# Optimization experiments

Hardware: AMD Instinct MI355X
Metric: run time of the kernel (lower is better)

## Reference

```python
import jax, jax.numpy as jnp
import numpy as np

B, C, N, H = 8, 256, 2048, 4
DIM = C // H
EPS = 1e-5
SLOPE = 0.2


def conv1x1(W, b, x):
    # W: [out, in], x: [B, in, N] -> [B, out, N]
    return jnp.einsum('oc,bcn->bon', W, x) + b[None, :, None]


def setup_inputs() -> dict:
    key = jax.random.key(0)
    ks = jax.random.split(key, 16)
    s = 1.0 / np.sqrt(C)
    s2 = 1.0 / np.sqrt(2 * C)
    return {
        'init_query': jax.random.normal(ks[0], (B, C, N), jnp.float32),
        'key': jax.random.normal(ks[1], (B, C, N), jnp.float32),
        'value': jax.random.normal(ks[2], (B, C, N), jnp.float32),
        'Wq': jax.random.normal(ks[3], (C, C), jnp.float32) * s,
        'bq': jax.random.normal(ks[4], (C,), jnp.float32) * s,
        'Wk': jax.random.normal(ks[5], (C, C), jnp.float32) * s,
        'bk': jax.random.normal(ks[6], (C,), jnp.float32) * s,
        'Wv': jax.random.normal(ks[7], (C, C), jnp.float32) * s,
        'bv': jax.random.normal(ks[8], (C,), jnp.float32) * s,
        'Wm': jax.random.normal(ks[9], (C, C), jnp.float32) * s,
        'bm': jax.random.normal(ks[10], (C,), jnp.float32) * s,
        'W1': jax.random.normal(ks[11], (2 * C, 2 * C), jnp.float32) * s2,
        'b1': jax.random.normal(ks[12], (2 * C,), jnp.float32) * s2,
        'gamma': jnp.ones((2 * C,), jnp.float32),
        'beta': jnp.zeros((2 * C,), jnp.float32),
        'W2': jax.random.normal(ks[13], (C, 2 * C), jnp.float32) * s2,
        'b2': jnp.zeros((C,), jnp.float32),  # nn.init.constant_(bias, 0.0)
    }


def reference(init_query, key, value, Wq, bq, Wk, bk, Wv, bv, Wm, bm, W1, b1, gamma, beta, W2, b2):
    # projections, then view [B, C, N] -> [B, dim, H, N] (dim outermost, matching torch .view)
    q = conv1x1(Wq, bq, init_query).reshape(B, DIM, H, N)
    k = conv1x1(Wk, bk, key).reshape(B, DIM, H, N)
    v = conv1x1(Wv, bv, value).reshape(B, DIM, H, N)
    scores = jnp.einsum('bdhn,bdhm->bhnm', q, k) / jnp.sqrt(jnp.float32(DIM))
    attn = jax.nn.softmax(scores, axis=-1)  # [B, H, N, N]
    x = jnp.einsum('bhnm,bdhm->bdhn', attn, v).reshape(B, C, N)
    x = conv1x1(Wm, bm, x)
    # post_merge: conv1x1 -> BatchNorm1d (training-mode batch stats) -> LeakyReLU(0.2) -> conv1x1
    h = conv1x1(W1, b1, jnp.concatenate([x, init_query], axis=1))  # [B, 2C, N]
    mu = jnp.mean(h, axis=(0, 2), keepdims=True)
    var = jnp.mean(jnp.square(h - mu), axis=(0, 2), keepdims=True)  # biased var, as torch BN
    hn = (h - mu) / jnp.sqrt(var + EPS) * gamma[None, :, None] + beta[None, :, None]
    hn = jnp.where(hn > 0, hn, SLOPE * hn)
    out = conv1x1(W2, b2, hn)
    return (out, attn)
```

## Files before the change

### kernel.cpp

```cpp
#include <hip/hip_runtime.h>
#include <stdint.h>

typedef __bf16 bf16x8 __attribute__((ext_vector_type(8)));
typedef float f32x4 __attribute__((ext_vector_type(4)));

constexpr int NB = 8;
constexpr int NC = 256;
constexpr int NN = 2048;
constexpr int NH = 4;
constexpr int ND = 64;
constexpr int NC2 = 512;
constexpr size_t TND = (size_t)NB * NN * NC;
__device__ constexpr float C2 = 0.125f * 1.4426950408889634f;

__device__ __forceinline__ ushort f2bf(float f) {
  union { float f; uint32_t u; } x; x.f = f;
  return (ushort)((x.u + 0x7FFFu + ((x.u >> 16) & 1u)) >> 16);
}
__device__ __forceinline__ float bf2f(ushort h) {
  union { uint32_t u; float f; } x; x.u = (uint32_t)h << 16;
  return x.f;
}

__device__ __forceinline__ void bar_lds() {
  __builtin_amdgcn_sched_barrier(0);
  asm volatile("s_waitcnt lgkmcnt(0)" ::: "memory");
  __builtin_amdgcn_s_barrier();
  __builtin_amdgcn_sched_barrier(0);
}


__global__ void k_cast_all(const float* __restrict__ Wq, const float* __restrict__ Wk,
                           const float* __restrict__ Wv, const float* __restrict__ Wm,
                           const float* __restrict__ W1, const float* __restrict__ W2,
                           ushort* __restrict__ wqkv, ushort* __restrict__ wm_b,
                           ushort* __restrict__ w1_b, ushort* __restrict__ w2_b) {
  int i = blockIdx.x * 256 + threadIdx.x;
  if (i < 196608) {
    int op = i >> 16, j = i & 65535;
    int r = j >> 8, c = j & 255;
    const float* s = op == 0 ? Wq : op == 1 ? Wk : Wv;
    int orig = op < 2 ? (((r & 63) << 2) | (r >> 6)) : r;
    wqkv[i] = f2bf(s[orig * NC + c]);
  } else if (i < 262144) {
    int j = i - 196608;
    int co = j >> 8, jj = j & 255;
    wm_b[j] = f2bf(Wm[co * NC + (jj & 63) * NH + (jj >> 6)]);
  } else if (i < 524288) {
    int j = i - 262144;
    w1_b[j] = f2bf(W1[j]);
  } else {
    int j = i - 524288;
    w2_b[j] = f2bf(W2[j]);
  }
}

__global__ void k_bn_finalize(const float* __restrict__ stats, const float* __restrict__ gamma,
                              const float* __restrict__ beta, float4* __restrict__ aff) {
  int c = blockIdx.x * 256 + threadIdx.x;
  if (c >= NC2) return;
  const float inv_n = 1.f / (float)(NB * NN);
  float mu  = stats[c * 2] * inv_n;
  float var = stats[c * 2 + 1] * inv_n - mu * mu;
  float isg = gamma[c] * rsqrtf(var + 1e-5f);
  aff[c] = make_float4(mu, isg, beta[c], 0.f);
}


__device__ __forceinline__ bf16x8 ldtile(const ushort* base, int lr, int lg, int fc, int ks) {
  int row = fc * 16 + lr;
  int u = (ks * 4 + lg) ^ (lr & 7);
  return *(const bf16x8*)((const char*)base + row * 128 + u * 16);
}

__global__ __launch_bounds__(256, 4) void k_attn(
    const ushort* __restrict__ qt, const ushort* __restrict__ kt,
    const ushort* __restrict__ vnat, float* __restrict__ attn,
    ushort* __restrict__ xT) {
  __shared__ ushort Kl[2][4096];
  __shared__ ushort Vl[2][4096];
  __shared__ ushort Pl[4096];

  const int tid = threadIdx.x;
  const int lane = tid & 63, w = tid >> 6;
  const int lr = lane & 15, lg = lane >> 4;

  int flat = blockIdx.x;
  int xcd = flat & 7, idx = flat >> 3;
  int z = xcd * 4 + (idx >> 5);
  int r0 = (idx & 31) * 64;
  int b = z >> 2, h = z & 3;

  const ushort* kbase = kt + (size_t)z * NN * ND;
  const ushort* vbase = vnat + ((size_t)b * NC + h) * NN;

  const int sr0 = tid >> 3, sc0 = tid & 7;
  const int sr1 = 32 + sr0;
  const int d0 = sr0 * 128 + ((sc0 ^ (sr0 & 7)) << 4);
  const int d1 = sr1 * 128 + ((sc0 ^ (sr1 & 7)) << 4);

  bf16x8 aq0, aq1;
  {
    const ushort* qp = qt + ((size_t)z * NN + r0 + w * 16 + lr) * ND;
    aq0 = *(const bf16x8*)(qp + lg * 8);
    aq1 = *(const bf16x8*)(qp + 32 + lg * 8);
  }

  uint4 gk0, gk1, gv0, gv1;

  gk0 = *(const uint4*)(kbase + (size_t)sr0 * ND + sc0 * 8);
  gk1 = *(const uint4*)(kbase + (size_t)sr1 * ND + sc0 * 8);
  *(uint4*)((char*)Kl[0] + d0) = gk0;
  *(uint4*)((char*)Kl[0] + d1) = gk1;
  gk0 = *(const uint4*)(kbase + (size_t)(64 + sr0) * ND + sc0 * 8);
  gk1 = *(const uint4*)(kbase + (size_t)(64 + sr1) * ND + sc0 * 8);
  bar_lds();

  float m_ln[4], s_ln[4];
#pragma unroll
  for (int j = 0; j < 4; ++j) { m_ln[j] = -INFINITY; s_ln[j] = 0.f; }

  for (int t = 0; t < 32; ++t) {
    int kb = t & 1;
    if (t < 31) {
      *(uint4*)((char*)Kl[kb ^ 1] + d0) = gk0;
      *(uint4*)((char*)Kl[kb ^ 1] + d1) = gk1;
    }
    if (t < 30) {
      gk0 = *(const uint4*)(kbase + ((size_t)(t + 2) * 64 + sr0) * ND + sc0 * 8);
      gk1 = *(const uint4*)(kbase + ((size_t)(t + 2) * 64 + sr1) * ND + sc0 * 8);
    }
    f32x4 sa[4] = {};
#pragma unroll
    for (int ks = 0; ks < 2; ++ks) {
      bf16x8 aqk = ks ? aq1 : aq0;
#pragma unroll
      for (int fc = 0; fc < 4; ++fc)
        sa[fc] = __builtin_amdgcn_mfma_f32_16x16x32_bf16(aqk, ldtile(Kl[kb], lr, lg, fc, ks), sa[fc], 0, 0, 0);
    }
#pragma unroll
    for (int j = 0; j < 4; ++j) {
      float tm = fmaxf(fmaxf(sa[0][j], sa[1][j]), fmaxf(sa[2][j], sa[3][j]));
      float mn = fmaxf(m_ln[j], tm);
      float mnC = mn * C2;
      float es = exp2f(fmaf(sa[0][j], C2, -mnC)) + exp2f(fmaf(sa[1][j], C2, -mnC))
               + exp2f(fmaf(sa[2][j], C2, -mnC)) + exp2f(fmaf(sa[3][j], C2, -mnC));
      s_ln[j] = s_ln[j] * exp2f(fmaf(m_ln[j], C2, -mnC)) + es;
      m_ln[j] = mn;
    }
    bar_lds();
  }

  float mC[4];
#pragma unroll
  for (int j = 0; j < 4; ++j) {
    float m = m_ln[j];
#pragma unroll
    for (int o = 1; o < 16; o <<= 1) m = fmaxf(m, __shfl_xor(m, o));
    float c = s_ln[j] * exp2f((m_ln[j] - m) * C2);
#pragma unroll
    for (int o = 1; o < 16; o <<= 1) c += __shfl_xor(c, o);
    mC[j] = m * C2 + __log2f(c);
  }

  gk0 = *(const uint4*)(kbase + (size_t)sr0 * ND + sc0 * 8);
  gk1 = *(const uint4*)(kbase + (size_t)sr1 * ND + sc0 * 8);
  gv0 = *(const uint4*)(vbase + (size_t)sr0 * 4 * NN + sc0 * 8);
  gv1 = *(const uint4*)(vbase + (size_t)sr1 * 4 * NN + sc0 * 8);
  *(uint4*)((char*)Kl[0] + d0) = gk0;
  *(uint4*)((char*)Kl[0] + d1) = gk1;
  *(uint4*)((char*)Vl[0] + d0) = gv0;
  *(uint4*)((char*)Vl[0] + d1) = gv1;
  gk0 = *(const uint4*)(kbase + (size_t)(64 + sr0) * ND + sc0 * 8);
  gk1 = *(const uint4*)(kbase + (size_t)(64 + sr1) * ND + sc0 * 8);
  gv0 = *(const uint4*)(vbase + (size_t)sr0 * 4 * NN + 64 + sc0 * 8);
  gv1 = *(const uint4*)(vbase + (size_t)sr1 * 4 * NN + 64 + sc0 * 8);
  bar_lds();

  f32x4 acc[4] = {};
  const int prow = w * 16 + lr;
  char* plb = (char*)Pl;
  for (int t = 0; t < 32; ++t) {
    int kb = t & 1;
    if (t < 31) {
      *(uint4*)((char*)Kl[kb ^ 1] + d0) = gk0;
      *(uint4*)((char*)Kl[kb ^ 1] + d1) = gk1;
      *(uint4*)((char*)Vl[kb ^ 1] + d0) = gv0;
      *(uint4*)((char*)Vl[kb ^ 1] + d1) = gv1;
    }
    if (t < 30) {
      gk0 = *(const uint4*)(kbase + ((size_t)(t + 2) * 64 + sr0) * ND + sc0 * 8);
      gk1 = *(const uint4*)(kbase + ((size_t)(t + 2) * 64 + sr1) * ND + sc0 * 8);
      gv0 = *(const uint4*)(vbase + (size_t)sr0 * 4 * NN + (t + 2) * 64 + sc0 * 8);
      gv1 = *(const uint4*)(vbase + (size_t)sr1 * 4 * NN + (t + 2) * 64 + sc0 * 8);
    }
    f32x4 sa[4] = {};
#pragma unroll
    for (int ks = 0; ks < 2; ++ks) {
      bf16x8 aqk = ks ? aq1 : aq0;
#pragma unroll
      for (int fc = 0; fc < 4; ++fc)
        sa[fc] = __builtin_amdgcn_mfma_f32_16x16x32_bf16(aqk, ldtile(Kl[kb], lr, lg, fc, ks), sa[fc], 0, 0, 0);
    }
#pragma unroll
    for (int fc = 0; fc < 4; ++fc)
#pragma unroll
      for (int j = 0; j < 4; ++j) {
        int row = w * 16 + lg * 4 + j;
        float p = exp2f(fmaf(sa[fc][j], C2, -mC[j]));
        int byte = (row << 7) + ((fc * 16 + lr) << 1);
        byte ^= (row & 7) << 4;
        *(ushort*)(plb + byte) = f2bf(p);
      }
    float* abase = attn + ((size_t)z * NN + r0) * NN + t * 64;
#pragma unroll
    for (int k = 0; k < 4; ++k) {
      int row = w * 16 + lg + k * 4;
      int byte = (row << 7) + (lr << 3);
      byte ^= (row & 7) << 4;
      const ushort* pq = (const ushort*)(plb + byte);
      f32x4 vv = { bf2f(pq[0]), bf2f(pq[1]), bf2f(pq[2]), bf2f(pq[3]) };
      __builtin_nontemporal_store(vv, (f32x4*)(abase + (size_t)row * NN + lr * 4));
    }
#pragma unroll
    for (int ks = 0; ks < 2; ++ks) {
      int abyte = (prow << 7) + ks * 64 + lg * 16;
      abyte ^= (prow & 7) << 4;
      bf16x8 ap = *(const bf16x8*)(plb + abyte);
#pragma unroll
      for (int fc = 0; fc < 4; ++fc)
        acc[fc] = __builtin_amdgcn_mfma_f32_16x16x32_bf16(ap, ldtile(Vl[kb], lr, lg, fc, ks), acc[fc], 0, 0, 0);
    }
    bar_lds();
  }
#pragma unroll
  for (int fc = 0; fc < 4; ++fc)
#pragma unroll
    for (int j = 0; j < 4; ++j) {
      int n = r0 + w * 16 + lg * 4 + j;
      xT[((size_t)b * NN + n) * NC + h * 64 + fc * 16 + lr] = f2bf(acc[fc][j]);
    }
}


enum GemmMode { M_PROJ = 0, M_WM, M_W1, M_W2 };

template <int MODE>
__global__ __launch_bounds__(256) void k_gemm(
    const ushort* __restrict__ A, const ushort* __restrict__ Bm,
    const float* __restrict__ Fa, const float* __restrict__ Fb, const float* __restrict__ Fc,
    const float* __restrict__ b0, const float* __restrict__ b1v, const float* __restrict__ b2v,
    const float4* __restrict__ aff, float* __restrict__ stats,
    float* __restrict__ outf, ushort* __restrict__ outb, ushort* __restrict__ outb2) {
  constexpr int BR = (MODE == M_WM || MODE == M_W2) ? 64 : 128;
  constexpr int BC = 128;
  constexpr int KT = (MODE == M_PROJ || MODE == M_WM) ? 256 : 512;
  constexpr int FR = BR / 32;
  constexpr int FC = 4;
  constexpr int LDL = 72;

  __shared__ ushort ldsU[BR * LDL + BC * LDL];
  ushort* ldsA = ldsU;
  ushort* ldsB = ldsU + BR * LDL;

  const int tid = threadIdx.x;
  const int lane = tid & 63, wave = tid >> 6;
  const int wr = (wave >> 1) * (FR * 16), wc = (wave & 1) * (FC * 16);
  const int lr = lane & 15, lg = lane >> 4, lk = lg * 8;
  const int c0 = blockIdx.x * BC, r0 = blockIdx.y * BR;
  const int op = (MODE == M_PROJ) ? (int)(blockIdx.z >> 3) : 0;
  const size_t z = (MODE == M_PROJ) ? (blockIdx.z & 7) : blockIdx.z;

  auto stage_t = [&](ushort* dst, const float* src) {
    int n = tid & 127, half = tid >> 7;
#pragma unroll
    for (int u = 0; u < 4; ++u) {
      int cg = half + u * 2;
      union { ushort us[8]; uint4 v; } pk;
#pragma unroll
      for (int e = 0; e < 8; ++e)
        pk.us[e] = f2bf(src[(size_t)(cg * 8 + e) * NN + n]);
      *(uint4*)&dst[n * LDL + cg * 8] = pk.v;
    }
  };

  f32x4 acc[FR][FC] = {};

  for (int kk = 0; kk < KT; kk += 64) {
    if constexpr (MODE == M_W1) {
      if (kk < NC) {
        const ushort* src = A + (z * NN + r0) * (size_t)NC + kk;
#pragma unroll
        for (int i = 0; i < BR / 32; ++i) {
          int off = (tid + i * 256) * 8, row = off >> 6, k = off & 63;
          *(uint4*)&ldsA[row * LDL + k] = *(const uint4*)(src + (size_t)row * NC + k);
        }
      } else {
        stage_t(ldsA, Fa + ((size_t)z * NC + (kk - NC)) * NN + r0);
      }
    } else {
      const ushort* src; int ld;
      if constexpr (MODE == M_PROJ)        { src = A + (size_t)op * NC * NC + (size_t)r0 * NC + kk; ld = NC; }
      else if constexpr (MODE == M_WM)     { src = A + (z * NN + r0) * (size_t)NC + kk; ld = NC; }
      else                                  { src = A + (size_t)r0 * NC2 + kk; ld = NC2; }
#pragma unroll
      for (int i = 0; i < BR / 32; ++i) {
        int off = (tid + i * 256) * 8, row = off >> 6, k = off & 63;
        *(uint4*)&ldsA[row * LDL + k] = *(const uint4*)(src + (size_t)row * ld + k);
      }
    }
    if constexpr (MODE == M_PROJ) {
      const float* Fsel = op == 0 ? Fa : op == 1 ? Fb : Fc;
      stage_t(ldsB, Fsel + ((size_t)z * NC + kk) * NN + c0);
    } else if constexpr (MODE == M_W2) {
      const ushort* src = Bm + (z * NN + c0) * (size_t)NC2 + kk;
#pragma unroll
      for (int i = 0; i < BC / 32; ++i) {
        int off = (tid + i * 256) * 8, row = off >> 6, k = off & 63;
        union { ushort u[8]; uint4 v; } t, o;
        t.v = *(const uint4*)(src + (size_t)row * NC2 + k);
#pragma unroll
        for (int e = 0; e < 8; ++e) {
          float4 pr = aff[kk + k + e];
          float y = (bf2f(t.u[e]) - pr.x) * pr.y + pr.z;
          y = y > 0.f ? y : 0.2f * y;
          o.u[e] = f2bf(y);
        }
        *(uint4*)&ldsB[row * LDL + k] = o.v;
      }
    } else {
      const ushort* src; int ld;
      if constexpr (MODE == M_WM)          { src = Bm + (size_t)c0 * NC + kk; ld = NC; }
      else                                  { src = Bm + (size_t)c0 * NC2 + kk; ld = NC2; }
#pragma unroll
      for (int i = 0; i < BC / 32; ++i) {
        int off = (tid + i * 256) * 8, row = off >> 6, k = off & 63;
        *(uint4*)&ldsB[row * LDL + k] = *(const uint4*)(src + (size_t)row * ld + k);
      }
    }
    __syncthreads();
#pragma unroll
    for (int ks = 0; ks < 2; ++ks) {
      bf16x8 afr[FR], bfr[FC];
#pragma unroll
      for (int fr = 0; fr < FR; ++fr)
        afr[fr] = *(const bf16x8*)&ldsA[(wr + fr * 16 + lr) * LDL + ks * 32 + lk];
#pragma unroll
      for (int fc = 0; fc < FC; ++fc)
        bfr[fc] = *(const bf16x8*)&ldsB[(wc + fc * 16 + lr) * LDL + ks * 32 + lk];
#pragma unroll
      for (int fr = 0; fr < FR; ++fr)
#pragma unroll
        for (int fc = 0; fc < FC; ++fc)
          acc[fr][fc] = __builtin_amdgcn_mfma_f32_16x16x32_bf16(afr[fr], bfr[fc], acc[fr][fc], 0, 0, 0);
    }
    __syncthreads();
  }

  if constexpr (MODE == M_PROJ) {
    if (op < 2) {
      const float* bb = op == 0 ? b0 : b1v;
      char* tb = (char*)ldsU;
#pragma unroll
      for (int fr = 0; fr < FR; ++fr)
#pragma unroll
        for (int fc = 0; fc < FC; ++fc) {
          int n_l = wc + fc * 16 + lr;
          int rb = wr + fr * 16 + lg * 4;
          union { ushort u[4]; uint2 v; } pk;
#pragma unroll
          for (int j = 0; j < 4; ++j) {
            int r = r0 + rb + j;
            pk.u[j] = f2bf(acc[fr][fc][j] + bb[((r & 63) << 2) | (r >> 6)]);
          }
          int byte = n_l * 256 + rb * 2;
          byte ^= (n_l & 7) << 4;
          *(uint2*)(tb + byte) = pk.v;
        }
      __syncthreads();
      ushort* dst = outb + (size_t)op * TND;
#pragma unroll
      for (int hh = 0; hh < 2; ++hh) {
        size_t zz = z * 4 + (r0 >> 6) + hh;
#pragma unroll
        for (int u = 0; u < 4; ++u) {
          int seg = u * 256 + tid;
          int n_l = seg >> 3, dd = (seg & 7) * 8;
          int byte = n_l * 256 + (hh * 64 + dd) * 2;
          byte ^= (n_l & 7) << 4;
          uint4 v = *(const uint4*)(tb + byte);
          *(uint4*)(dst + (zz * NN + c0 + n_l) * (size_t)ND + dd) = v;
        }
      }
    } else {
#pragma unroll
      for (int fr = 0; fr < FR; ++fr)
#pragma unroll
        for (int fc = 0; fc < FC; ++fc)
#pragma unroll
          for (int j = 0; j < 4; ++j) {
            int r = r0 + wr + fr * 16 + lg * 4 + j;
            int c = c0 + wc + fc * 16 + lr;
            outb2[(z * NC + r) * (size_t)NN + c] = f2bf(acc[fr][fc][j] + b2v[r]);
          }
    }
    return;
  }

  float sfc[FC], qfc[FC];
#pragma unroll
  for (int fc = 0; fc < FC; ++fc) { sfc[fc] = 0.f; qfc[fc] = 0.f; }
#pragma unroll
  for (int fr = 0; fr < FR; ++fr)
#pragma unroll
    for (int fc = 0; fc < FC; ++fc)
#pragma unroll
      for (int j = 0; j < 4; ++j) {
        int r = r0 + wr + fr * 16 + lg * 4 + j;
        int c = c0 + wc + fc * 16 + lr;
        float v = acc[fr][fc][j];
        if constexpr (MODE == M_WM) {
          v += b0[c];
          outb[(z * NN + r) * (size_t)NC + c] = f2bf(v);
        } else if constexpr (MODE == M_W1) {
          v += b0[c];
          outb[(z * NN + r) * (size_t)NC2 + c] = f2bf(v);
          sfc[fc] += v; qfc[fc] += v * v;
        } else {
          v += b0[r];
          outf[(z * NC + r) * (size_t)NN + c] = v;
        }
      }
  if constexpr (MODE == M_W1) {
#pragma unroll
    for (int fc = 0; fc < FC; ++fc) {
      float s1 = sfc[fc], s2 = qfc[fc];
      s1 += __shfl_xor(s1, 16); s1 += __shfl_xor(s1, 32);
      s2 += __shfl_xor(s2, 16); s2 += __shfl_xor(s2, 32);
      if (lane < 16) {
        int ch = c0 + wc + fc * 16 + lane;
        atomicAdd(&stats[ch * 2],     s1);
        atomicAdd(&stats[ch * 2 + 1], s2);
      }
    }
  }
}


extern "C" void kernel_launch(void* const* d_in, const int* in_sizes, int n_in,
                              void* d_out, int out_size, void* d_ws, size_t ws_size,
                              hipStream_t stream) {
  const float* iq    = (const float*)d_in[0];
  const float* keyi  = (const float*)d_in[1];
  const float* vali  = (const float*)d_in[2];
  const float* Wq = (const float*)d_in[3];  const float* bq = (const float*)d_in[4];
  const float* Wk = (const float*)d_in[5];  const float* bk = (const float*)d_in[6];
  const float* Wv = (const float*)d_in[7];  const float* bv = (const float*)d_in[8];
  const float* Wm = (const float*)d_in[9];  const float* bm = (const float*)d_in[10];
  const float* W1 = (const float*)d_in[11]; const float* b1 = (const float*)d_in[12];
  const float* gamma = (const float*)d_in[13]; const float* beta = (const float*)d_in[14];
  const float* W2 = (const float*)d_in[15]; const float* b2 = (const float*)d_in[16];

  float* out  = (float*)d_out;
  float* attn = out + (size_t)NB * NC * NN;

  uint8_t* cur = (uint8_t*)d_ws;
  auto alloc = [&](size_t bytes) { uint8_t* p = cur; cur += (bytes + 255) & ~(size_t)255; return p; };
  ushort* wqkv  = (ushort*)alloc((size_t)NC * NC * 2 * 3);
  ushort* wm_b  = (ushort*)alloc((size_t)NC * NC * 2);
  ushort* w1_b  = (ushort*)alloc((size_t)NC2 * NC2 * 2);
  ushort* w2_b  = (ushort*)alloc((size_t)NC * NC2 * 2);
  ushort* qtkt  = (ushort*)alloc(TND * 2 * 2);
  ushort* v_nat = (ushort*)alloc(TND * 2);
  ushort* xT    = (ushort*)alloc(TND * 2);
  ushort* xmT   = (ushort*)alloc(TND * 2);
  ushort* hT    = (ushort*)alloc((size_t)NB * NN * NC2 * 2);
  float*  stats = (float*)alloc(NC2 * 2 * 4);
  float4* aff   = (float4*)alloc(NC2 * 16);
  ushort* kt    = qtkt + TND;

  (void)hipMemsetAsync(stats, 0, NC2 * 2 * 4, stream);

  k_cast_all<<<dim3(2560), 256, 0, stream>>>(Wq, Wk, Wv, Wm, W1, W2, wqkv, wm_b, w1_b, w2_b);

  k_gemm<M_PROJ><<<dim3(16, 2, 24), 256, 0, stream>>>(
      wqkv, nullptr, iq, keyi, vali, bq, bk, bv, nullptr, nullptr, nullptr, qtkt, v_nat);

  k_attn<<<dim3(1024), 256, 0, stream>>>(qtkt, kt, v_nat, attn, xT);

  k_gemm<M_WM><<<dim3(2, 32, 8), 256, 0, stream>>>(
      xT, wm_b, nullptr, nullptr, nullptr, bm, nullptr, nullptr, nullptr, nullptr, nullptr, xmT, nullptr);

  k_gemm<M_W1><<<dim3(4, 16, 8), 256, 0, stream>>>(
      xmT, w1_b, iq, nullptr, nullptr, b1, nullptr, nullptr, nullptr, stats, nullptr, hT, nullptr);

  k_bn_finalize<<<dim3(2), 256, 0, stream>>>(stats, gamma, beta, aff);

  k_gemm<M_W2><<<dim3(16, 4, 8), 256, 0, stream>>>(
      w2_b, hT, nullptr, nullptr, nullptr, b2, nullptr, nullptr, aff, nullptr, out, nullptr, nullptr);
}
```

Baseline: 266.4 us.

## Fold merge conv into first post-merge conv and fuse BN finalize into W2 GEMM

Precomputes W1[:, :C] @ Wm (with the head permutation) and the folded bias in the prep kernel, so the separate Wm GEMM over all activations and its intermediate buffer are removed. The BN finalize kernel is dropped: each W2 GEMM block recomputes the per-channel affine from stats into shared memory. This saves one full GEMM pass, a round trip to memory and two launches. In exchange the prep kernel does a small matmul serially per thread, every W2 block repeats the finalize work, and the folded weights are rounded to bf16 directly rather than applied in two steps.

```diff
diff --git a/kernel.cpp b/kernel.cpp
--- a/kernel.cpp
+++ b/kernel.cpp
@@ -30,40 +30,45 @@
 }
 
 
-__global__ void k_cast_all(const float* __restrict__ Wq, const float* __restrict__ Wk,
-                           const float* __restrict__ Wv, const float* __restrict__ Wm,
-                           const float* __restrict__ W1, const float* __restrict__ W2,
-                           ushort* __restrict__ wqkv, ushort* __restrict__ wm_b,
-                           ushort* __restrict__ w1_b, ushort* __restrict__ w2_b) {
-  int i = blockIdx.x * 256 + threadIdx.x;
-  if (i < 196608) {
-    int op = i >> 16, j = i & 65535;
-    int r = j >> 8, c = j & 255;
-    const float* s = op == 0 ? Wq : op == 1 ? Wk : Wv;
-    int orig = op < 2 ? (((r & 63) << 2) | (r >> 6)) : r;
-    wqkv[i] = f2bf(s[orig * NC + c]);
-  } else if (i < 262144) {
-    int j = i - 196608;
-    int co = j >> 8, jj = j & 255;
-    wm_b[j] = f2bf(Wm[co * NC + (jj & 63) * NH + (jj >> 6)]);
-  } else if (i < 524288) {
-    int j = i - 262144;
-    w1_b[j] = f2bf(W1[j]);
+__global__ void k_prep(const float* __restrict__ Wq, const float* __restrict__ Wk,
+                       const float* __restrict__ Wv, const float* __restrict__ Wm,
+                       const float* __restrict__ W1, const float* __restrict__ W2,
+                       const float* __restrict__ bm, const float* __restrict__ b1,
+                       ushort* __restrict__ wqkv, ushort* __restrict__ w2_b,
+                       ushort* __restrict__ wf_b, float* __restrict__ bias_f) {
+  int blk = blockIdx.x, tid = threadIdx.x;
+  if (blk < 1792) {
+    int gid = blk * 256 + tid;
+    if (gid < 196608) {
+      int op = gid >> 16, j = gid & 65535;
+      int r = j >> 8, c = j & 255;
+      const float* s = op == 0 ? Wq : op == 1 ? Wk : Wv;
+      int orig = op < 2 ? (((r & 63) << 2) | (r >> 6)) : r;
+      wqkv[gid] = f2bf(s[orig * NC + c]);
+    } else if (gid < 327680) {
+      int j = gid - 196608;
+      w2_b[j] = f2bf(W2[j]);
+    } else {
+      int j = gid - 327680;
+      int o = j >> 8, co = j & 255;
+      wf_b[o * NC2 + NC + co] = f2bf(W1[o * NC2 + NC + co]);
+    }
   } else {
-    int j = i - 524288;
-    w2_b[j] = f2bf(W2[j]);
-  }
-}
-
-__global__ void k_bn_finalize(const float* __restrict__ stats, const float* __restrict__ gamma,
-                              const float* __restrict__ beta, float4* __restrict__ aff) {
-  int c = blockIdx.x * 256 + threadIdx.x;
-  if (c >= NC2) return;
-  const float inv_n = 1.f / (float)(NB * NN);
-  float mu  = stats[c * 2] * inv_n;
-  float var = stats[c * 2 + 1] * inv_n - mu * mu;
-  float isg = gamma[c] * rsqrtf(var + 1e-5f);
-  aff[c] = make_float4(mu, isg, beta[c], 0.f);
+    int o = blk - 1792;
+    int pc = ((tid & 63) << 2) | (tid >> 6);
+    const float* w1row = W1 + (size_t)o * NC2;
+    float acc = 0.f;
+    for (int co = 0; co < NC; ++co)
+      acc = fmaf(w1row[co], Wm[co * NC + pc], acc);
+    wf_b[o * NC2 + tid] = f2bf(acc);
+    float pb = w1row[tid] * bm[tid];
+#pragma unroll
+    for (int ofs = 1; ofs < 64; ofs <<= 1) pb += __shfl_xor(pb, ofs);
+    __shared__ float red[4];
+    if ((tid & 63) == 0) red[tid >> 6] = pb;
+    __syncthreads();
+    if (tid == 0) bias_f[o] = b1[o] + red[0] + red[1] + red[2] + red[3];
+  }
 }
 
 
@@ -243,23 +248,24 @@
 }
 
 
-enum GemmMode { M_PROJ = 0, M_WM, M_W1, M_W2 };
+enum GemmMode { M_PROJ = 0, M_W1, M_W2 };
 
 template <int MODE>
 __global__ __launch_bounds__(256) void k_gemm(
     const ushort* __restrict__ A, const ushort* __restrict__ Bm,
     const float* __restrict__ Fa, const float* __restrict__ Fb, const float* __restrict__ Fc,
     const float* __restrict__ b0, const float* __restrict__ b1v, const float* __restrict__ b2v,
-    const float4* __restrict__ aff, float* __restrict__ stats,
+    float* __restrict__ stats,
     float* __restrict__ outf, ushort* __restrict__ outb, ushort* __restrict__ outb2) {
-  constexpr int BR = (MODE == M_WM || MODE == M_W2) ? 64 : 128;
+  constexpr int BR = (MODE == M_W2) ? 64 : 128;
   constexpr int BC = 128;
-  constexpr int KT = (MODE == M_PROJ || MODE == M_WM) ? 256 : 512;
+  constexpr int KT = (MODE == M_PROJ) ? 256 : 512;
   constexpr int FR = BR / 32;
   constexpr int FC = 4;
   constexpr int LDL = 72;
 
   __shared__ ushort ldsU[BR * LDL + BC * LDL];
+  __shared__ float4 affl[(MODE == M_W2) ? NC2 : 1];
   ushort* ldsA = ldsU;
   ushort* ldsB = ldsU + BR * LDL;
 
@@ -271,6 +277,17 @@
   const int op = (MODE == M_PROJ) ? (int)(blockIdx.z >> 3) : 0;
   const size_t z = (MODE == M_PROJ) ? (blockIdx.z & 7) : blockIdx.z;
 
+  if constexpr (MODE == M_W2) {
+    const float inv_n = 1.f / (float)(NB * NN);
+    for (int c = tid; c < NC2; c += 256) {
+      float mu  = stats[c * 2] * inv_n;
+      float var = stats[c * 2 + 1] * inv_n - mu * mu;
+      float isg = b1v[c] * rsqrtf(var + 1e-5f);
+      affl[c] = make_float4(mu, isg, b2v[c], 0.f);
+    }
+    __syncthreads();
+  }
+
   auto stage_t = [&](ushort* dst, const float* src) {
     int n = tid & 127, half = tid >> 7;
 #pragma unroll
@@ -300,9 +317,8 @@
       }
     } else {
       const ushort* src; int ld;
-      if constexpr (MODE == M_PROJ)        { src = A + (size_t)op * NC * NC + (size_t)r0 * NC + kk; ld = NC; }
-      else if constexpr (MODE == M_WM)     { src = A + (z * NN + r0) * (size_t)NC + kk; ld = NC; }
-      else                                  { src = A + (size_t)r0 * NC2 + kk; ld = NC2; }
+      if constexpr (MODE == M_PROJ) { src = A + (size_t)op * NC * NC + (size_t)r0 * NC + kk; ld = NC; }
+      else                           { src = A + (size_t)r0 * NC2 + kk; ld = NC2; }
 #pragma unroll
       for (int i = 0; i < BR / 32; ++i) {
         int off = (tid + i * 256) * 8, row = off >> 6, k = off & 63;
@@ -321,7 +337,7 @@
         t.v = *(const uint4*)(src + (size_t)row * NC2 + k);
 #pragma unroll
         for (int e = 0; e < 8; ++e) {
-          float4 pr = aff[kk + k + e];
+          float4 pr = affl[kk + k + e];
           float y = (bf2f(t.u[e]) - pr.x) * pr.y + pr.z;
           y = y > 0.f ? y : 0.2f * y;
           o.u[e] = f2bf(y);
@@ -329,13 +345,11 @@
         *(uint4*)&ldsB[row * LDL + k] = o.v;
       }
     } else {
-      const ushort* src; int ld;
-      if constexpr (MODE == M_WM)          { src = Bm + (size_t)c0 * NC + kk; ld = NC; }
-      else                                  { src = Bm + (size_t)c0 * NC2 + kk; ld = NC2; }
+      const ushort* src = Bm + (size_t)c0 * NC2 + kk;
 #pragma unroll
       for (int i = 0; i < BC / 32; ++i) {
         int off = (tid + i * 256) * 8, row = off >> 6, k = off & 63;
-        *(uint4*)&ldsB[row * LDL + k] = *(const uint4*)(src + (size_t)row * ld + k);
+        *(uint4*)&ldsB[row * LDL + k] = *(const uint4*)(src + (size_t)row * NC2 + k);
       }
     }
     __syncthreads();
@@ -419,10 +433,7 @@
         int r = r0 + wr + fr * 16 + lg * 4 + j;
         int c = c0 + wc + fc * 16 + lr;
         float v = acc[fr][fc][j];
-        if constexpr (MODE == M_WM) {
-          v += b0[c];
-          outb[(z * NN + r) * (size_t)NC + c] = f2bf(v);
-        } else if constexpr (MODE == M_W1) {
+        if constexpr (MODE == M_W1) {
           v += b0[c];
           outb[(z * NN + r) * (size_t)NC2 + c] = f2bf(v);
           sfc[fc] += v; qfc[fc] += v * v;
@@ -466,36 +477,30 @@
 
   uint8_t* cur = (uint8_t*)d_ws;
   auto alloc = [&](size_t bytes) { uint8_t* p = cur; cur += (bytes + 255) & ~(size_t)255; return p; };
-  ushort* wqkv  = (ushort*)alloc((size_t)NC * NC * 2 * 3);
-  ushort* wm_b  = (ushort*)alloc((size_t)NC * NC * 2);
-  ushort* w1_b  = (ushort*)alloc((size_t)NC2 * NC2 * 2);
-  ushort* w2_b  = (ushort*)alloc((size_t)NC * NC2 * 2);
-  ushort* qtkt  = (ushort*)alloc(TND * 2 * 2);
-  ushort* v_nat = (ushort*)alloc(TND * 2);
-  ushort* xT    = (ushort*)alloc(TND * 2);
-  ushort* xmT   = (ushort*)alloc(TND * 2);
-  ushort* hT    = (ushort*)alloc((size_t)NB * NN * NC2 * 2);
-  float*  stats = (float*)alloc(NC2 * 2 * 4);
-  float4* aff   = (float4*)alloc(NC2 * 16);
-  ushort* kt    = qtkt + TND;
+  ushort* wqkv   = (ushort*)alloc((size_t)NC * NC * 2 * 3);
+  ushort* w2_b   = (ushort*)alloc((size_t)NC * NC2 * 2);
+  ushort* wf_b   = (ushort*)alloc((size_t)NC2 * NC2 * 2);
+  float*  bias_f = (float*)alloc(NC2 * 4);
+  ushort* qtkt   = (ushort*)alloc(TND * 2 * 2);
+  ushort* v_nat  = (ushort*)alloc(TND * 2);
+  ushort* xT     = (ushort*)alloc(TND * 2);
+  ushort* hT     = (ushort*)alloc((size_t)NB * NN * NC2 * 2);
+  float*  stats  = (float*)alloc(NC2 * 2 * 4);
+  ushort* kt     = qtkt + TND;
 
   (void)hipMemsetAsync(stats, 0, NC2 * 2 * 4, stream);
 
-  k_cast_all<<<dim3(2560), 256, 0, stream>>>(Wq, Wk, Wv, Wm, W1, W2, wqkv, wm_b, w1_b, w2_b);
+  k_prep<<<dim3(2304), 256, 0, stream>>>(Wq, Wk, Wv, Wm, W1, W2, bm, b1,
+                                         wqkv, w2_b, wf_b, bias_f);
 
   k_gemm<M_PROJ><<<dim3(16, 2, 24), 256, 0, stream>>>(
-      wqkv, nullptr, iq, keyi, vali, bq, bk, bv, nullptr, nullptr, nullptr, qtkt, v_nat);
+      wqkv, nullptr, iq, keyi, vali, bq, bk, bv, nullptr, nullptr, qtkt, v_nat);
 
   k_attn<<<dim3(1024), 256, 0, stream>>>(qtkt, kt, v_nat, attn, xT);
 
-  k_gemm<M_WM><<<dim3(2, 32, 8), 256, 0, stream>>>(
-      xT, wm_b, nullptr, nullptr, nullptr, bm, nullptr, nullptr, nullptr, nullptr, nullptr, xmT, nullptr);
-
   k_gemm<M_W1><<<dim3(4, 16, 8), 256, 0, stream>>>(
-      xmT, w1_b, iq, nullptr, nullptr, b1, nullptr, nullptr, nullptr, stats, nullptr, hT, nullptr);
-
-  k_bn_finalize<<<dim3(2), 256, 0, stream>>>(stats, gamma, beta, aff);
+      xT, wf_b, iq, nullptr, nullptr, bias_f, nullptr, nullptr, stats, nullptr, hT, nullptr);
 
   k_gemm<M_W2><<<dim3(16, 4, 8), 256, 0, stream>>>(
-      w2_b, hT, nullptr, nullptr, nullptr, b2, nullptr, nullptr, aff, nullptr, out, nullptr, nullptr);
-}
+      w2_b, hT, nullptr, nullptr, nullptr, b2, gamma, beta, stats, out, nullptr, nullptr);
+}
```

Measured after the change: 324.0 us. 21.6% more time.
